# Kernel tuning notes

Measured on AMD Instinct MI355X. Metric: run time of the kernel, lower is better.

Reference implementation:

```python
import jax, jax.numpy as jnp
import numpy as np

B, S = 128, 32
C = [4, 8, 16, 32]
DN = ('NDHWC', 'DHWIO', 'NDHWC')


def _conv(x, w, stride=1, pad=None):
    k = w.shape[0]
    if pad is None:
        pad = [((k - 1) // 2, k // 2)] * 3  # k=3 -> (1,1); k=4 -> (1,2) as in scn even-kernel convention
    return jax.lax.conv_general_dilated(x, w, (stride,) * 3, pad, dimension_numbers=DN)


def _bn_relu(x, g, b, mask, eps=1e-4):
    # BatchNormLeakyReLU with leakiness=0 (ReLU); stats over ACTIVE voxels only, per channel
    cnt = jnp.maximum(mask.sum(), 1.0)
    mean = (x * mask).sum(axis=(0, 1, 2, 3)) / cnt
    var = (((x - mean) ** 2) * mask).sum(axis=(0, 1, 2, 3)) / cnt
    y = (x - mean) * jax.lax.rsqrt(var + eps) * g + b
    return jnp.maximum(y, 0.0) * mask


def _pool_mask(m):
    # scn.Convolution k=2 s=2: output site active iff any input in its 2^3 receptive field is active
    return jax.lax.reduce_window(m, 0.0, jax.lax.max, (1, 2, 2, 2, 1), (1, 2, 2, 2, 1), 'VALID')


def _up_mask(m):
    # scn.FullConvolution k=2 s=2: each active input activates its full 2^3 output block
    return jnp.repeat(jnp.repeat(jnp.repeat(m, 2, 1), 2, 2), 2, 3)


def _encoder(vox, maskraw, wp, enc, dec, wo):
    mask = (maskraw == 0).astype(vox.dtype)
    x = vox * mask
    x = _conv(x, wp) * mask  # prepare: submanifold conv 1 -> m=4
    for (g, b, ws, wd) in enc:  # 3 non-empty encoding stages (i < num_strides-1)
        x = _bn_relu(x, g, b, mask)
        x = _conv(x, ws) * mask               # submanifold conv k=3
        x = _conv(x, wd, stride=2, pad=[(0, 0)] * 3)  # strided Convolution k=2 s=2
        mask = _pool_mask(mask)
        x = x * mask
    # SparseToDense + view(-1, C*s^3) in NCDHW layout
    hidden = jnp.transpose(x, (0, 4, 1, 2, 3)).reshape(x.shape[0], -1)
    for (g, b, wu, ws3, ws4) in dec:  # i = 2, 1, 0
        x = _bn_relu(x, g, b, mask)
        x = jax.lax.conv_transpose(x, wu, (2, 2, 2), 'VALID', dimension_numbers=DN)  # FullConvolution
        mask = _up_mask(mask)
        x = x * mask
        x = _conv(x, ws3) * mask              # submanifold conv k=3 (end of decoding_conv1)
        mask = mask * (x[..., :1] > 0).astype(x.dtype)  # SparsifyFCS (applied twice; idempotent)
        x = x * mask
        x = _conv(x, ws4) * mask              # submanifold conv k=4 (decoding_conv2)
    out = _conv(x, wo) * mask                 # output: submanifold conv m -> 1
    return hidden, out


def setup_inputs():
    key = jax.random.key(0)
    ks = iter(jax.random.split(key, 64))

    def rnd(shape, s=0.1):
        return jax.random.normal(next(ks), shape, jnp.float32) * s

    inp = {}
    inp['vox'] = jax.random.normal(next(ks), (B, S, S, S, 1), jnp.float32)
    inp['maskraw'] = jax.random.randint(next(ks), (B, S, S, S, 1), 0, 10, jnp.int32)
    inp['wp'] = rnd((3, 3, 3, 1, C[0]))
    for i in range(3):
        ci, co = C[i], C[i + 1]
        inp[f'g_e{i}'] = 1.0 + rnd((ci,))
        inp[f'b_e{i}'] = rnd((ci,))
        inp[f'ws_e{i}'] = rnd((3, 3, 3, ci, ci))
        inp[f'wd_e{i}'] = rnd((2, 2, 2, ci, co))
    for j, i in enumerate([2, 1, 0]):
        ci, co = C[i + 1], C[i]
        inp[f'g_d{j}'] = 1.0 + rnd((ci,))
        inp[f'b_d{j}'] = rnd((ci,))
        inp[f'wu_d{j}'] = rnd((2, 2, 2, ci, co))
        inp[f'ws3_d{j}'] = rnd((3, 3, 3, co, co))
        inp[f'ws4_d{j}'] = rnd((4, 4, 4, co, co))
    inp['wo'] = rnd((3, 3, 3, C[0], 1))
    return inp


def reference(vox, maskraw, wp, g_e0, b_e0, ws_e0, wd_e0, g_e1, b_e1, ws_e1, wd_e1, g_e2, b_e2, ws_e2, wd_e2, g_d0, b_d0, wu_d0, ws3_d0, ws4_d0, g_d1, b_d1, wu_d1, ws3_d1, ws4_d1, g_d2, b_d2, wu_d2, ws3_d2, ws4_d2, wo):
    enc = [(g_e0, b_e0, ws_e0, wd_e0), (g_e1, b_e1, ws_e1, wd_e1), (g_e2, b_e2, ws_e2, wd_e2)]
    dec = [(g_d0, b_d0, wu_d0, ws3_d0, ws4_d0), (g_d1, b_d1, wu_d1, ws3_d1, ws4_d1), (g_d2, b_d2, wu_d2, ws3_d2, ws4_d2)]
    return _encoder(vox, maskraw, wp, enc, dec, wo)
```

## Files before the change

### kernel.cpp

```cpp
#include <hip/hip_runtime.h>

using u8 = unsigned char;

__global__ void mask_init_k(const int* __restrict__ mr, u8* __restrict__ m, int N) {
    int i = blockIdx.x * blockDim.x + threadIdx.x;
    if (i < N) m[i] = (mr[i] == 0) ? 1 : 0;
}

template <int SO>
__global__ void pool_k(const u8* __restrict__ mi, u8* __restrict__ mo) {
    const int N = 128 * SO * SO * SO;
    constexpr int SI = 2 * SO;
    int v = blockIdx.x * blockDim.x + threadIdx.x;
    if (v >= N) return;
    int t = v;
    int x = t % SO; t /= SO;
    int y = t % SO; t /= SO;
    int z = t % SO;
    int n = t / SO;
    u8 m = 0;
    for (int kd = 0; kd < 2; kd++)
        for (int kh = 0; kh < 2; kh++)
            for (int kw = 0; kw < 2; kw++)
                m |= mi[((n * SI + 2 * z + kd) * SI + 2 * y + kh) * SI + 2 * x + kw];
    mo[v] = m;
}


__global__ void prep4t_k(const float* __restrict__ vox, const u8* __restrict__ m,
                         const float* __restrict__ wp, float* __restrict__ out) {
    __shared__ float til[6 * 10 * 35];
    int bid = blockIdx.x;
    int y0 = (bid & 3) << 3, z0 = ((bid >> 2) & 7) << 2, n = bid >> 5;
    for (int t = threadIdx.x; t < 6 * 10 * 35; t += 256) {
        int x_ = t % 35;
        int rr = t / 35;
        int yy = rr % 10, zz = rr / 10;
        int gx = x_ - 1, gy = y0 + yy - 1, gz = z0 + zz - 1;
        float v = 0.f;
        if ((unsigned)gx < 32u && (unsigned)gy < 32u && (unsigned)gz < 32u) {
            int gi = ((n * 32 + gz) * 32 + gy) * 32 + gx;
            if (m[gi]) v = vox[gi];
        }
        til[t] = v;
    }
    __syncthreads();
    int tx = threadIdx.x;
    int xg = tx & 7, ly = (tx >> 3) & 7, lz = tx >> 6;
    int xb = xg << 2;
    int vbase = ((n * 32 + z0 + lz) * 32 + y0 + ly) * 32 + xb;
    u8 om[4];
#pragma unroll
    for (int j = 0; j < 4; j++) om[j] = m[vbase + j];
    float acc[4][4];
#pragma unroll
    for (int j = 0; j < 4; j++)
#pragma unroll
        for (int co = 0; co < 4; co++) acc[j][co] = 0.f;
    for (int kd = 0; kd < 3; kd++) {
        for (int kh = 0; kh < 3; kh++) {
            const float* rowp = &til[((lz + kd) * 10 + ly + kh) * 35 + xb];
            float col[6];
#pragma unroll
            for (int c = 0; c < 6; c++) col[c] = rowp[c];
            const float* wrow = wp + ((kd * 3 + kh) * 3) * 4;
#pragma unroll
            for (int kw = 0; kw < 3; kw++) {
                const float* wt = wrow + kw * 4;
#pragma unroll
                for (int j = 0; j < 4; j++) {
                    float xv = col[j + kw];
#pragma unroll
                    for (int co = 0; co < 4; co++) acc[j][co] += xv * wt[co];
                }
            }
        }
    }
#pragma unroll
    for (int j = 0; j < 4; j++)
#pragma unroll
        for (int co = 0; co < 4; co++)
            out[(size_t)(vbase + j) * 4 + co] = om[j] ? acc[j][co] : 0.f;
}

__global__ void convbn4t_k(const float* __restrict__ in, const float* __restrict__ w,
                           const u8* __restrict__ mask, const double* __restrict__ params,
                           float* __restrict__ out) {
    __shared__ float4 til[6 * 10 * 35];
    float sc[4], sh[4];
#pragma unroll
    for (int c = 0; c < 4; c++) { sc[c] = (float)params[c]; sh[c] = (float)params[4 + c]; }
    int bid = blockIdx.x;
    int y0 = (bid & 3) << 3, z0 = ((bid >> 2) & 7) << 2, n = bid >> 5;
    for (int t = threadIdx.x; t < 6 * 10 * 35; t += 256) {
        int x_ = t % 35;
        int rr = t / 35;
        int yy = rr % 10, zz = rr / 10;
        int gx = x_ - 1, gy = y0 + yy - 1, gz = z0 + zz - 1;
        float4 v = make_float4(0.f, 0.f, 0.f, 0.f);
        if ((unsigned)gx < 32u && (unsigned)gy < 32u && (unsigned)gz < 32u) {
            int gi = ((n * 32 + gz) * 32 + gy) * 32 + gx;
            if (mask[gi]) {
                float4 r = *(const float4*)(in + (size_t)gi * 4);
                v.x = fmaxf(r.x * sc[0] + sh[0], 0.f);
                v.y = fmaxf(r.y * sc[1] + sh[1], 0.f);
                v.z = fmaxf(r.z * sc[2] + sh[2], 0.f);
                v.w = fmaxf(r.w * sc[3] + sh[3], 0.f);
            }
        }
        til[t] = v;
    }
    __syncthreads();
    int tx = threadIdx.x;
    int xg = tx & 7, ly = (tx >> 3) & 7, lz = tx >> 6;
    int xb = xg << 2;
    int vbase = ((n * 32 + z0 + lz) * 32 + y0 + ly) * 32 + xb;
    u8 om[4];
#pragma unroll
    for (int j = 0; j < 4; j++) om[j] = mask[vbase + j];
    float acc[4][4];
#pragma unroll
    for (int j = 0; j < 4; j++)
#pragma unroll
        for (int co = 0; co < 4; co++) acc[j][co] = 0.f;
    for (int kd = 0; kd < 3; kd++) {
        for (int kh = 0; kh < 3; kh++) {
            const float4* rowp = &til[((lz + kd) * 10 + ly + kh) * 35 + xb];
            float col[6][4];
#pragma unroll
            for (int c = 0; c < 6; c++) {
                float4 t4 = rowp[c];
                col[c][0] = t4.x; col[c][1] = t4.y; col[c][2] = t4.z; col[c][3] = t4.w;
            }
            const float* wrow = w + ((kd * 3 + kh) * 3) * 16;
#pragma unroll
            for (int kw = 0; kw < 3; kw++) {
                const float* wt = wrow + kw * 16;
#pragma unroll
                for (int j = 0; j < 4; j++) {
#pragma unroll
                    for (int ci = 0; ci < 4; ci++) {
                        float xv = col[j + kw][ci];
#pragma unroll
                        for (int co = 0; co < 4; co++) acc[j][co] += xv * wt[ci * 4 + co];
                    }
                }
            }
        }
    }
#pragma unroll
    for (int j = 0; j < 4; j++)
#pragma unroll
        for (int co = 0; co < 4; co++)
            out[(size_t)(vbase + j) * 4 + co] = om[j] ? acc[j][co] : 0.f;
}

__global__ void conv3s4t_k(const float* __restrict__ in, const float* __restrict__ w,
                           const u8* __restrict__ pmask, u8* __restrict__ nmask,
                           float* __restrict__ out, double delta) {
    __shared__ float4 til[6 * 10 * 35];
    int bid = blockIdx.x;
    int y0 = (bid & 3) << 3, z0 = ((bid >> 2) & 7) << 2, n = bid >> 5;
    for (int t = threadIdx.x; t < 6 * 10 * 35; t += 256) {
        int x_ = t % 35;
        int rr = t / 35;
        int yy = rr % 10, zz = rr / 10;
        int gx = x_ - 1, gy = y0 + yy - 1, gz = z0 + zz - 1;
        float4 v = make_float4(0.f, 0.f, 0.f, 0.f);
        if ((unsigned)gx < 32u && (unsigned)gy < 32u && (unsigned)gz < 32u)
            v = *(const float4*)(in + (size_t)(((n * 32 + gz) * 32 + gy) * 32 + gx) * 4);
        til[t] = v;
    }
    __syncthreads();
    int tx = threadIdx.x;
    int xg = tx & 7, ly = (tx >> 3) & 7, lz = tx >> 6;
    int xb = xg << 2;
    int gy = y0 + ly, gz = z0 + lz;
    int vbase = ((n * 32 + gz) * 32 + gy) * 32 + xb;
    int pbase = ((n * 16 + (gz >> 1)) * 16 + (gy >> 1)) * 16 + (xb >> 1);
    u8 pm[4];
    pm[0] = pm[1] = pmask[pbase];
    pm[2] = pm[3] = pmask[pbase + 1];
    double acc0[4], asum[4];
    float accf[4][4];
#pragma unroll
    for (int j = 0; j < 4; j++) {
        acc0[j] = 0.0; asum[j] = 0.0;
#pragma unroll
        for (int co = 0; co < 4; co++) accf[j][co] = 0.f;
    }
    for (int kd = 0; kd < 3; kd++) {
        for (int kh = 0; kh < 3; kh++) {
            const float4* rowp = &til[((lz + kd) * 10 + ly + kh) * 35 + xb];
            float col[6][4];
#pragma unroll
            for (int c = 0; c < 6; c++) {
                float4 t4 = rowp[c];
                col[c][0] = t4.x; col[c][1] = t4.y; col[c][2] = t4.z; col[c][3] = t4.w;
            }
            const float* wrow = w + ((kd * 3 + kh) * 3) * 16;
#pragma unroll
            for (int kw = 0; kw < 3; kw++) {
                const float* wt = wrow + kw * 16;
#pragma unroll
                for (int j = 0; j < 4; j++) {
#pragma unroll
                    for (int ci = 0; ci < 4; ci++) {
                        float xv = col[j + kw][ci];
                        double term = (double)xv * (double)wt[ci * 4 + 0];
                        acc0[j] += term;
                        asum[j] += fabs(term);
#pragma unroll
                        for (int co = 1; co < 4; co++) accf[j][co] += xv * wt[ci * 4 + co];
                    }
                }
            }
        }
    }
#pragma unroll
    for (int j = 0; j < 4; j++) {
        u8 nm = (pm[j] && (acc0[j] > -delta * asum[j])) ? 1 : 0;
        nmask[vbase + j] = nm;
        out[(size_t)(vbase + j) * 4 + 0] = nm ? (float)acc0[j] : 0.f;
#pragma unroll
        for (int co = 1; co < 4; co++) out[(size_t)(vbase + j) * 4 + co] = nm ? accf[j][co] : 0.f;
    }
}

__global__ void conv4x4t_k(const float* __restrict__ in, const float* __restrict__ w,
                           const u8* __restrict__ outmask, float* __restrict__ out) {
    __shared__ float4 til[7 * 11 * 35];
    int bid = blockIdx.x;
    int y0 = (bid & 3) << 3, z0 = ((bid >> 2) & 7) << 2, n = bid >> 5;
    for (int t = threadIdx.x; t < 7 * 11 * 35; t += 256) {
        int x_ = t % 35;
        int rr = t / 35;
        int yy = rr % 11, zz = rr / 11;
        int gx = x_ - 1, gy = y0 + yy - 1, gz = z0 + zz - 1;
        float4 v = make_float4(0.f, 0.f, 0.f, 0.f);
        if ((unsigned)gx < 32u && (unsigned)gy < 32u && (unsigned)gz < 32u)
            v = *(const float4*)(in + (size_t)(((n * 32 + gz) * 32 + gy) * 32 + gx) * 4);
        til[t] = v;
    }
    __syncthreads();
    int tx = threadIdx.x;
    int xg = tx & 7, ly = (tx >> 3) & 7, lz = tx >> 6;
    int xb = xg << 2;
    int vbase = ((n * 32 + z0 + lz) * 32 + y0 + ly) * 32 + xb;
    u8 om[4];
#pragma unroll
    for (int j = 0; j < 4; j++) om[j] = outmask[vbase + j];
    float acc[4][4];
#pragma unroll
    for (int j = 0; j < 4; j++)
#pragma unroll
        for (int co = 0; co < 4; co++) acc[j][co] = 0.f;
    for (int kd = 0; kd < 4; kd++) {
        for (int kh = 0; kh < 4; kh++) {
            const float4* rowp = &til[((lz + kd) * 11 + ly + kh) * 35 + xb];
            float col[7][4];
#pragma unroll
            for (int c = 0; c < 7; c++) {
                float4 t4 = rowp[c];
                col[c][0] = t4.x; col[c][1] = t4.y; col[c][2] = t4.z; col[c][3] = t4.w;
            }
            const float* wrow = w + ((kd * 4 + kh) * 4) * 16;
#pragma unroll
            for (int kw = 0; kw < 4; kw++) {
                const float* wt = wrow + kw * 16;
#pragma unroll
                for (int j = 0; j < 4; j++) {
#pragma unroll
                    for (int ci = 0; ci < 4; ci++) {
                        float xv = col[j + kw][ci];
#pragma unroll
                        for (int co = 0; co < 4; co++) acc[j][co] += xv * wt[ci * 4 + co];
                    }
                }
            }
        }
    }
#pragma unroll
    for (int j = 0; j < 4; j++)
#pragma unroll
        for (int co = 0; co < 4; co++)
            out[(size_t)(vbase + j) * 4 + co] = om[j] ? acc[j][co] : 0.f;
}

__global__ void outconv4t_k(const float* __restrict__ in, const float* __restrict__ w,
                            const u8* __restrict__ mask, float* __restrict__ out) {
    __shared__ float4 til[6 * 10 * 35];
    int bid = blockIdx.x;
    int y0 = (bid & 3) << 3, z0 = ((bid >> 2) & 7) << 2, n = bid >> 5;
    for (int t = threadIdx.x; t < 6 * 10 * 35; t += 256) {
        int x_ = t % 35;
        int rr = t / 35;
        int yy = rr % 10, zz = rr / 10;
        int gx = x_ - 1, gy = y0 + yy - 1, gz = z0 + zz - 1;
        float4 v = make_float4(0.f, 0.f, 0.f, 0.f);
        if ((unsigned)gx < 32u && (unsigned)gy < 32u && (unsigned)gz < 32u)
            v = *(const float4*)(in + (size_t)(((n * 32 + gz) * 32 + gy) * 32 + gx) * 4);
        til[t] = v;
    }
    __syncthreads();
    int tx = threadIdx.x;
    int xg = tx & 7, ly = (tx >> 3) & 7, lz = tx >> 6;
    int xb = xg << 2;
    int vbase = ((n * 32 + z0 + lz) * 32 + y0 + ly) * 32 + xb;
    u8 om[4];
#pragma unroll
    for (int j = 0; j < 4; j++) om[j] = mask[vbase + j];
    float acc[4] = {0.f, 0.f, 0.f, 0.f};
    for (int kd = 0; kd < 3; kd++) {
        for (int kh = 0; kh < 3; kh++) {
            const float4* rowp = &til[((lz + kd) * 10 + ly + kh) * 35 + xb];
            float col[6][4];
#pragma unroll
            for (int c = 0; c < 6; c++) {
                float4 t4 = rowp[c];
                col[c][0] = t4.x; col[c][1] = t4.y; col[c][2] = t4.z; col[c][3] = t4.w;
            }
            const float* wrow = w + ((kd * 3 + kh) * 3) * 4;
#pragma unroll
            for (int kw = 0; kw < 3; kw++) {
                const float* wt = wrow + kw * 4;
#pragma unroll
                for (int j = 0; j < 4; j++) {
#pragma unroll
                    for (int ci = 0; ci < 4; ci++) acc[j] += col[j + kw][ci] * wt[ci];
                }
            }
        }
    }
#pragma unroll
    for (int j = 0; j < 4; j++) out[vbase + j] = om[j] ? acc[j] : 0.f;
}


template <int K, int CIN, int COUT, int S>
__global__ void conv_k(const float* __restrict__ in, const float* __restrict__ w,
                       const u8* __restrict__ outmask, float* __restrict__ out) {
    const int N = 128 * S * S * S;
    int v = blockIdx.x * blockDim.x + threadIdx.x;
    if (v >= N) return;
    if (!outmask[v]) {
#pragma unroll
        for (int co = 0; co < COUT; co++) out[(size_t)v * COUT + co] = 0.f;
        return;
    }
    int t = v;
    int x = t % S; t /= S;
    int y = t % S; t /= S;
    int z = t % S;
    int n = t / S;
    float acc[COUT];
#pragma unroll
    for (int co = 0; co < COUT; co++) acc[co] = 0.f;
    constexpr int PLO = (K - 1) / 2;
    for (int kd = 0; kd < K; kd++) {
        int zz = z + kd - PLO; if ((unsigned)zz >= (unsigned)S) continue;
        for (int kh = 0; kh < K; kh++) {
            int yy = y + kh - PLO; if ((unsigned)yy >= (unsigned)S) continue;
            for (int kw = 0; kw < K; kw++) {
                int xx = x + kw - PLO; if ((unsigned)xx >= (unsigned)S) continue;
                int sv = ((n * S + zz) * S + yy) * S + xx;
                const float* ip = in + (size_t)sv * CIN;
                const float* wpk = w + ((kd * K + kh) * K + kw) * CIN * COUT;
#pragma unroll
                for (int ci = 0; ci < CIN; ci++) {
                    float xv = ip[ci];
#pragma unroll
                    for (int co = 0; co < COUT; co++) acc[co] += xv * wpk[ci * COUT + co];
                }
            }
        }
    }
#pragma unroll
    for (int co = 0; co < COUT; co++) out[(size_t)v * COUT + co] = acc[co];
}

template <int CIN, int COUT, int S>
__global__ void convbn_k(const float* __restrict__ in, const float* __restrict__ w,
                         const u8* __restrict__ mask, const double* __restrict__ params,
                         float* __restrict__ out) {
    const int N = 128 * S * S * S;
    int v = blockIdx.x * blockDim.x + threadIdx.x;
    if (v >= N) return;
    if (!mask[v]) {
#pragma unroll
        for (int co = 0; co < COUT; co++) out[(size_t)v * COUT + co] = 0.f;
        return;
    }
    int t = v;
    int x = t % S; t /= S;
    int y = t % S; t /= S;
    int z = t % S;
    int n = t / S;
    float sc[CIN], sh[CIN];
#pragma unroll
    for (int c = 0; c < CIN; c++) { sc[c] = (float)params[c]; sh[c] = (float)params[CIN + c]; }
    float acc[COUT];
#pragma unroll
    for (int co = 0; co < COUT; co++) acc[co] = 0.f;
    for (int kd = 0; kd < 3; kd++) {
        int zz = z + kd - 1; if ((unsigned)zz >= (unsigned)S) continue;
        for (int kh = 0; kh < 3; kh++) {
            int yy = y + kh - 1; if ((unsigned)yy >= (unsigned)S) continue;
            for (int kw = 0; kw < 3; kw++) {
                int xx = x + kw - 1; if ((unsigned)xx >= (unsigned)S) continue;
                int sv = ((n * S + zz) * S + yy) * S + xx;
                if (!mask[sv]) continue;
                const float* ip = in + (size_t)sv * CIN;
                const float* wpk = w + ((kd * 3 + kh) * 3 + kw) * CIN * COUT;
#pragma unroll
                for (int ci = 0; ci < CIN; ci++) {
                    float yv = fmaxf(ip[ci] * sc[ci] + sh[ci], 0.f);
#pragma unroll
                    for (int co = 0; co < COUT; co++) acc[co] += yv * wpk[ci * COUT + co];
                }
            }
        }
    }
#pragma unroll
    for (int co = 0; co < COUT; co++) out[(size_t)v * COUT + co] = acc[co];
}

template <int CIN, int COUT, int S>
__global__ void conv3s_k(const float* __restrict__ in, const float* __restrict__ w,
                         const u8* __restrict__ pmask, u8* __restrict__ nmask,
                         float* __restrict__ out, double delta) {
    const int N = 128 * S * S * S;
    constexpr int SP = S / 2;
    int v = blockIdx.x * blockDim.x + threadIdx.x;
    if (v >= N) return;
    int t = v;
    int x = t % S; t /= S;
    int y = t % S; t /= S;
    int z = t % S;
    int n = t / S;
    int pidx = ((n * SP + (z >> 1)) * SP + (y >> 1)) * SP + (x >> 1);
    if (!pmask[pidx]) {
        nmask[v] = 0;
#pragma unroll
        for (int co = 0; co < COUT; co++) out[(size_t)v * COUT + co] = 0.f;
        return;
    }
    double acc0 = 0.0, asum = 0.0;
    float acc[COUT];
#pragma unroll
    for (int co = 0; co < COUT; co++) acc[co] = 0.f;
    for (int kd = 0; kd < 3; kd++) {
        int zz = z + kd - 1; if ((unsigned)zz >= (unsigned)S) continue;
        for (int kh = 0; kh < 3; kh++) {
            int yy = y + kh - 1; if ((unsigned)yy >= (unsigned)S) continue;
            for (int kw = 0; kw < 3; kw++) {
                int xx = x + kw - 1; if ((unsigned)xx >= (unsigned)S) continue;
                int sv = ((n * S + zz) * S + yy) * S + xx;
                const float* ip = in + (size_t)sv * CIN;
                const float* wpk = w + ((kd * 3 + kh) * 3 + kw) * CIN * COUT;
#pragma unroll
                for (int ci = 0; ci < CIN; ci++) {
                    float xv = ip[ci];
                    double term = (double)xv * (double)wpk[ci * COUT + 0];
                    acc0 += term;
                    asum += fabs(term);
#pragma unroll
                    for (int co = 1; co < COUT; co++) acc[co] += xv * wpk[ci * COUT + co];
                }
            }
        }
    }
    u8 nm = (acc0 > -delta * asum) ? 1 : 0;
    nmask[v] = nm;
    out[(size_t)v * COUT + 0] = nm ? (float)acc0 : 0.f;
#pragma unroll
    for (int co = 1; co < COUT; co++) out[(size_t)v * COUT + co] = nm ? acc[co] : 0.f;
}

template <int CIN, int COUT, int SO>
__global__ void down_k(const float* __restrict__ in, const float* __restrict__ w,
                       const u8* __restrict__ outmask, float* __restrict__ out) {
    const int N = 128 * SO * SO * SO;
    constexpr int SI = 2 * SO;
    int v = blockIdx.x * blockDim.x + threadIdx.x;
    if (v >= N) return;
    if (!outmask[v]) {
#pragma unroll
        for (int co = 0; co < COUT; co++) out[(size_t)v * COUT + co] = 0.f;
        return;
    }
    int t = v;
    int x = t % SO; t /= SO;
    int y = t % SO; t /= SO;
    int z = t % SO;
    int n = t / SO;
    float acc[COUT];
#pragma unroll
    for (int co = 0; co < COUT; co++) acc[co] = 0.f;
    for (int kd = 0; kd < 2; kd++)
        for (int kh = 0; kh < 2; kh++)
            for (int kw = 0; kw < 2; kw++) {
                int sv = ((n * SI + 2 * z + kd) * SI + 2 * y + kh) * SI + 2 * x + kw;
                const float* ip = in + (size_t)sv * CIN;
                const float* wpk = w + ((kd * 2 + kh) * 2 + kw) * CIN * COUT;
#pragma unroll
                for (int ci = 0; ci < CIN; ci++) {
                    float xv = ip[ci];
#pragma unroll
                    for (int co = 0; co < COUT; co++) acc[co] += xv * wpk[ci * COUT + co];
                }
            }
#pragma unroll
    for (int co = 0; co < COUT; co++) out[(size_t)v * COUT + co] = acc[co];
}

template <int CIN, int COUT, int SI>
__global__ void upbn_k(const float* __restrict__ in, const float* __restrict__ w,
                       const u8* __restrict__ inmask, const double* __restrict__ params,
                       float* __restrict__ out) {
    constexpr int SO = 2 * SI;
    const int N = 128 * SO * SO * SO;
    int v = blockIdx.x * blockDim.x + threadIdx.x;
    if (v >= N) return;
    int t = v;
    int x = t % SO; t /= SO;
    int y = t % SO; t /= SO;
    int z = t % SO;
    int n = t / SO;
    int sv = ((n * SI + (z >> 1)) * SI + (y >> 1)) * SI + (x >> 1);
    if (!inmask[sv]) {
#pragma unroll
        for (int co = 0; co < COUT; co++) out[(size_t)v * COUT + co] = 0.f;
        return;
    }
    int tap = ((1 - (z & 1)) * 2 + (1 - (y & 1))) * 2 + (1 - (x & 1));
    const float* wpk = w + tap * CIN * COUT;
    const float* ip = in + (size_t)sv * CIN;
    float acc[COUT];
#pragma unroll
    for (int co = 0; co < COUT; co++) acc[co] = 0.f;
#pragma unroll
    for (int ci = 0; ci < CIN; ci++) {
        float yv = fmaxf(ip[ci] * (float)params[ci] + (float)params[CIN + ci], 0.f);
#pragma unroll
        for (int co = 0; co < COUT; co++) acc[co] += yv * wpk[ci * COUT + co];
    }
#pragma unroll
    for (int co = 0; co < COUT; co++) out[(size_t)v * COUT + co] = acc[co];
}

template <int C>
__global__ void bn_reduce_k(const float* __restrict__ x, const u8* __restrict__ m, int N,
                            double* __restrict__ partial) {
    double cnt = 0.0, sx[C], s2[C];
#pragma unroll
    for (int c = 0; c < C; c++) { sx[c] = 0.0; s2[c] = 0.0; }
    int stride = gridDim.x * blockDim.x;
    for (int v = blockIdx.x * blockDim.x + threadIdx.x; v < N; v += stride) {
        if (!m[v]) continue;
        cnt += 1.0;
#pragma unroll
        for (int c = 0; c < C; c++) {
            double xv = (double)x[(size_t)v * C + c];
            sx[c] += xv;
            s2[c] += xv * xv;
        }
    }
#pragma unroll
    for (int off = 32; off > 0; off >>= 1) {
        cnt += __shfl_down(cnt, off, 64);
#pragma unroll
        for (int c = 0; c < C; c++) {
            sx[c] += __shfl_down(sx[c], off, 64);
            s2[c] += __shfl_down(s2[c], off, 64);
        }
    }
    __shared__ double sbuf[4][2 * C + 1];
    int wave = threadIdx.x >> 6;
    if ((threadIdx.x & 63) == 0) {
        sbuf[wave][0] = cnt;
#pragma unroll
        for (int c = 0; c < C; c++) {
            sbuf[wave][1 + c] = sx[c];
            sbuf[wave][1 + C + c] = s2[c];
        }
    }
    __syncthreads();
    if (threadIdx.x == 0) {
        double* p = partial + (size_t)blockIdx.x * (2 * C + 1);
        double tcnt = 0.0;
        for (int wv = 0; wv < 4; wv++) tcnt += sbuf[wv][0];
        p[0] = tcnt;
#pragma unroll
        for (int c = 0; c < C; c++) {
            double a = 0.0, b = 0.0;
            for (int wv = 0; wv < 4; wv++) { a += sbuf[wv][1 + c]; b += sbuf[wv][1 + C + c]; }
            p[1 + c] = a;
            p[1 + C + c] = b;
        }
    }
}

template <int C>
__global__ void bn_final_k(const double* __restrict__ partial, int nblocks,
                           const float* __restrict__ g, const float* __restrict__ b,
                           double* __restrict__ params) {
    int c = threadIdx.x;
    if (c >= C) return;
    double cnt = 0.0, sx = 0.0, s2 = 0.0;
    for (int bk = 0; bk < nblocks; bk++) {
        const double* p = partial + (size_t)bk * (2 * C + 1);
        cnt += p[0];
        sx += p[1 + c];
        s2 += p[1 + C + c];
    }
    if (cnt < 1.0) cnt = 1.0;
    double mean = sx / cnt;
    double var = s2 / cnt - mean * mean;
    double sc = (double)g[c] / sqrt(var + 1e-4);
    params[c] = sc;
    params[C + c] = (double)b[c] - mean * sc;
}

__global__ void hidden_k(const float* __restrict__ x, float* __restrict__ out) {
    int i = blockIdx.x * blockDim.x + threadIdx.x;
    if (i >= 128 * 2048) return;
    int b = i >> 11;
    int r = i & 2047;
    int c = r >> 6;
    int s = r & 63;
    int d = s >> 4;
    int h = (s >> 2) & 3;
    int w = s & 3;
    out[i] = x[((((b * 4 + d) * 4 + h) * 4 + w) << 5) + c];
}

extern "C" void kernel_launch(void* const* d_in, const int* in_sizes, int n_in,
                              void* d_out, int out_size, void* d_ws, size_t ws_size,
                              hipStream_t stream) {
    const float* vox = (const float*)d_in[0];
    const int* mraw = (const int*)d_in[1];
    const float* wp = (const float*)d_in[2];
    const float* g_e0 = (const float*)d_in[3];
    const float* b_e0 = (const float*)d_in[4];
    const float* ws_e0 = (const float*)d_in[5];
    const float* wd_e0 = (const float*)d_in[6];
    const float* g_e1 = (const float*)d_in[7];
    const float* b_e1 = (const float*)d_in[8];
    const float* ws_e1 = (const float*)d_in[9];
    const float* wd_e1 = (const float*)d_in[10];
    const float* g_e2 = (const float*)d_in[11];
    const float* b_e2 = (const float*)d_in[12];
    const float* ws_e2 = (const float*)d_in[13];
    const float* wd_e2 = (const float*)d_in[14];
    const float* g_d0 = (const float*)d_in[15];
    const float* b_d0 = (const float*)d_in[16];
    const float* wu_d0 = (const float*)d_in[17];
    const float* ws3_d0 = (const float*)d_in[18];
    const float* ws4_d0 = (const float*)d_in[19];
    const float* g_d1 = (const float*)d_in[20];
    const float* b_d1 = (const float*)d_in[21];
    const float* wu_d1 = (const float*)d_in[22];
    const float* ws3_d1 = (const float*)d_in[23];
    const float* ws4_d1 = (const float*)d_in[24];
    const float* g_d2 = (const float*)d_in[25];
    const float* b_d2 = (const float*)d_in[26];
    const float* wu_d2 = (const float*)d_in[27];
    const float* ws3_d2 = (const float*)d_in[28];
    const float* ws4_d2 = (const float*)d_in[29];
    const float* wo = (const float*)d_in[30];
    float* out = (float*)d_out;

    float* wsf = (float*)d_ws;
    size_t offf = 0;
    auto allocf = [&](size_t n) { float* p = wsf + offf; offf += n; return p; };
    float* R1 = allocf(16777216);
    float* R2 = allocf(16777216);
    float* S1 = allocf(1048576);
    float* S2 = allocf(1048576);
    float* T = allocf(262144);
    double* wsd = (double*)(wsf + offf);
    double* partial = wsd;
    double* params = wsd + 16640;
    u8* wsm = (u8*)(wsd + 16640 + 128);
    size_t offm = 0;
    auto allocm = [&](size_t n) { u8* p = wsm + offm; offm += n; return p; };
    u8* m32 = allocm(4194304);
    u8* m16 = allocm(524288);
    u8* m8 = allocm(65536);
    u8* m4 = allocm(8192);
    u8* mD8 = allocm(65536);
    u8* mD16 = allocm(524288);
    u8* mD32 = allocm(4194304);

    const int N32 = 128 * 32768;
    const int N16 = 128 * 4096;
    const int N8 = 128 * 512;
    const int N4 = 128 * 64;
    auto gs = [](int n) { return dim3((n + 255) / 256); };
    auto rbn = [](int n) { int bl = (n + 255) / 256; return bl > 256 ? 256 : bl; };
    dim3 blk(256);
    dim3 tgrid(4096);

    mask_init_k<<<gs(N32), blk, 0, stream>>>(mraw, m32, N32);
    pool_k<16><<<gs(N16), blk, 0, stream>>>(m32, m16);
    pool_k<8><<<gs(N8), blk, 0, stream>>>(m16, m8);
    pool_k<4><<<gs(N4), blk, 0, stream>>>(m8, m4);

    prep4t_k<<<tgrid, blk, 0, stream>>>(vox, m32, wp, R1);
    int nb0 = rbn(N32);
    bn_reduce_k<4><<<dim3(nb0), blk, 0, stream>>>(R1, m32, N32, partial);
    bn_final_k<4><<<1, 64, 0, stream>>>(partial, nb0, g_e0, b_e0, params);
    convbn4t_k<<<tgrid, blk, 0, stream>>>(R1, ws_e0, m32, params, R2);
    down_k<4, 8, 16><<<gs(N16), blk, 0, stream>>>(R2, wd_e0, m16, R1);

    int nb1 = rbn(N16);
    bn_reduce_k<8><<<dim3(nb1), blk, 0, stream>>>(R1, m16, N16, partial);
    bn_final_k<8><<<1, 64, 0, stream>>>(partial, nb1, g_e1, b_e1, params);
    convbn_k<8, 8, 16><<<gs(N16), blk, 0, stream>>>(R1, ws_e1, m16, params, R2);
    down_k<8, 16, 8><<<gs(N8), blk, 0, stream>>>(R2, wd_e1, m8, S1);

    int nb2 = rbn(N8);
    bn_reduce_k<16><<<dim3(nb2), blk, 0, stream>>>(S1, m8, N8, partial);
    bn_final_k<16><<<1, 64, 0, stream>>>(partial, nb2, g_e2, b_e2, params);
    convbn_k<16, 16, 8><<<gs(N8), blk, 0, stream>>>(S1, ws_e2, m8, params, S2);
    down_k<16, 32, 4><<<gs(N4), blk, 0, stream>>>(S2, wd_e2, m4, T);

    hidden_k<<<gs(128 * 2048), blk, 0, stream>>>(T, out);

    int nb3 = rbn(N4);
    bn_reduce_k<32><<<dim3(nb3), blk, 0, stream>>>(T, m4, N4, partial);
    bn_final_k<32><<<1, 64, 0, stream>>>(partial, nb3, g_d0, b_d0, params);
    upbn_k<32, 16, 4><<<gs(N8), blk, 0, stream>>>(T, wu_d0, m4, params, S1);
    conv3s_k<16, 16, 8><<<gs(N8), blk, 0, stream>>>(S1, ws3_d0, m4, mD8, S2, 4e-7);
    conv_k<4, 16, 16, 8><<<gs(N8), blk, 0, stream>>>(S2, ws4_d0, mD8, S1);

    int nb4 = rbn(N8);
    bn_reduce_k<16><<<dim3(nb4), blk, 0, stream>>>(S1, mD8, N8, partial);
    bn_final_k<16><<<1, 64, 0, stream>>>(partial, nb4, g_d1, b_d1, params);
    upbn_k<16, 8, 8><<<gs(N16), blk, 0, stream>>>(S1, wu_d1, mD8, params, R1);
    conv3s_k<8, 8, 16><<<gs(N16), blk, 0, stream>>>(R1, ws3_d1, mD8, mD16, R2, 4e-7);
    conv_k<4, 8, 8, 16><<<gs(N16), blk, 0, stream>>>(R2, ws4_d1, mD16, R1);

    int nb5 = rbn(N16);
    bn_reduce_k<8><<<dim3(nb5), blk, 0, stream>>>(R1, mD16, N16, partial);
    bn_final_k<8><<<1, 64, 0, stream>>>(partial, nb5, g_d2, b_d2, params);
    upbn_k<8, 4, 16><<<gs(N32), blk, 0, stream>>>(R1, wu_d2, mD16, params, R2);
    conv3s4t_k<<<tgrid, blk, 0, stream>>>(R2, ws3_d2, mD16, mD32, R1, 0.0);
    conv4x4t_k<<<tgrid, blk, 0, stream>>>(R1, ws4_d2, mD32, R2);
    outconv4t_k<<<tgrid, blk, 0, stream>>>(R2, wo, mD32, out + 262144);
}
```

Measured before the change: 1.455 ms.

## Tile 8^3-resolution 16-channel convolutions through shared memory per z-slice

Replaces the three 16-channel convolutions at 8^3 resolution (encoder conv with fused BN+ReLU, decoder k=3 sparsify conv, decoder k=4 conv) with kernels that stage a haloed z-slab of input into LDS. Each 64-thread block then computes one 8x8 z-plane from the shared tile instead of every voxel gathering its neighbours from global memory. This cuts redundant global reads, but it also removes the early exit for masked-out voxels, so every voxel now does the full MAC work. The small 64-thread blocks may also limit occupancy and latency hiding.

Result: slower. 1.576 ms (+8.3%).

```diff
diff --git a/kernel.cpp b/kernel.cpp
--- a/kernel.cpp
+++ b/kernel.cpp
@@ -334,6 +334,160 @@
     }
 #pragma unroll
     for (int j = 0; j < 4; j++) out[vbase + j] = om[j] ? acc[j] : 0.f;
+}
+
+
+__global__ void convbn8_k(const float* __restrict__ in, const float* __restrict__ w,
+                          const u8* __restrict__ mask, const double* __restrict__ params,
+                          float* __restrict__ out) {
+    __shared__ float til[3 * 10 * 11 * 16];
+    float sc[16], sh[16];
+#pragma unroll
+    for (int c = 0; c < 16; c++) { sc[c] = (float)params[c]; sh[c] = (float)params[16 + c]; }
+    int z = blockIdx.x & 7, n = blockIdx.x >> 3;
+    for (int t = threadIdx.x; t < 300; t += 64) {
+        int xx = t % 10;
+        int rr = t / 10;
+        int yy = rr % 10, zz = rr / 10;
+        int gx = xx - 1, gy = yy - 1, gz = z + zz - 1;
+        float v[16];
+#pragma unroll
+        for (int c = 0; c < 16; c++) v[c] = 0.f;
+        if ((unsigned)gx < 8u && (unsigned)gy < 8u && (unsigned)gz < 8u) {
+            int gi = ((n * 8 + gz) * 8 + gy) * 8 + gx;
+            if (mask[gi]) {
+                const float* ip = in + (size_t)gi * 16;
+#pragma unroll
+                for (int c = 0; c < 16; c++) v[c] = fmaxf(ip[c] * sc[c] + sh[c], 0.f);
+            }
+        }
+        float* dst = &til[((zz * 10 + yy) * 11 + xx) * 16];
+#pragma unroll
+        for (int k = 0; k < 4; k++)
+            ((float4*)dst)[k] = make_float4(v[4 * k], v[4 * k + 1], v[4 * k + 2], v[4 * k + 3]);
+    }
+    __syncthreads();
+    int x = threadIdx.x & 7, y = threadIdx.x >> 3;
+    int v = ((n * 8 + z) * 8 + y) * 8 + x;
+    u8 om = mask[v];
+    float acc[16];
+#pragma unroll
+    for (int co = 0; co < 16; co++) acc[co] = 0.f;
+    for (int kd = 0; kd < 3; kd++) {
+        for (int kh = 0; kh < 3; kh++) {
+            const float* rp = &til[((kd * 10 + (y + kh)) * 11 + x) * 16];
+#pragma unroll
+            for (int kw = 0; kw < 3; kw++) {
+                const float* xp = rp + kw * 16;
+                const float* wt = w + ((kd * 3 + kh) * 3 + kw) * 256;
+#pragma unroll
+                for (int ci = 0; ci < 16; ci++) {
+                    float xv = xp[ci];
+#pragma unroll
+                    for (int co = 0; co < 16; co++) acc[co] += xv * wt[ci * 16 + co];
+                }
+            }
+        }
+    }
+#pragma unroll
+    for (int co = 0; co < 16; co++) out[(size_t)v * 16 + co] = om ? acc[co] : 0.f;
+}
+
+__global__ void conv3s8_k(const float* __restrict__ in, const float* __restrict__ w,
+                          const u8* __restrict__ pmask, u8* __restrict__ nmask,
+                          float* __restrict__ out, double delta) {
+    __shared__ float til[3 * 10 * 11 * 16];
+    int z = blockIdx.x & 7, n = blockIdx.x >> 3;
+    for (int t = threadIdx.x; t < 300; t += 64) {
+        int xx = t % 10;
+        int rr = t / 10;
+        int yy = rr % 10, zz = rr / 10;
+        int gx = xx - 1, gy = yy - 1, gz = z + zz - 1;
+        float4 v0 = make_float4(0.f, 0.f, 0.f, 0.f), v1 = v0, v2 = v0, v3 = v0;
+        if ((unsigned)gx < 8u && (unsigned)gy < 8u && (unsigned)gz < 8u) {
+            const float4* ip = (const float4*)(in + (size_t)(((n * 8 + gz) * 8 + gy) * 8 + gx) * 16);
+            v0 = ip[0]; v1 = ip[1]; v2 = ip[2]; v3 = ip[3];
+        }
+        float4* dst = (float4*)&til[((zz * 10 + yy) * 11 + xx) * 16];
+        dst[0] = v0; dst[1] = v1; dst[2] = v2; dst[3] = v3;
+    }
+    __syncthreads();
+    int x = threadIdx.x & 7, y = threadIdx.x >> 3;
+    int v = ((n * 8 + z) * 8 + y) * 8 + x;
+    int pidx = ((n * 4 + (z >> 1)) * 4 + (y >> 1)) * 4 + (x >> 1);
+    u8 pm = pmask[pidx];
+    double acc0 = 0.0, asum = 0.0;
+    float accf[16];
+#pragma unroll
+    for (int co = 0; co < 16; co++) accf[co] = 0.f;
+    for (int kd = 0; kd < 3; kd++) {
+        for (int kh = 0; kh < 3; kh++) {
+            const float* rp = &til[((kd * 10 + (y + kh)) * 11 + x) * 16];
+#pragma unroll
+            for (int kw = 0; kw < 3; kw++) {
+                const float* xp = rp + kw * 16;
+                const float* wt = w + ((kd * 3 + kh) * 3 + kw) * 256;
+#pragma unroll
+                for (int ci = 0; ci < 16; ci++) {
+                    float xv = xp[ci];
+                    double term = (double)xv * (double)wt[ci * 16 + 0];
+                    acc0 += term;
+                    asum += fabs(term);
+#pragma unroll
+                    for (int co = 1; co < 16; co++) accf[co] += xv * wt[ci * 16 + co];
+                }
+            }
+        }
+    }
+    u8 nm = (pm && (acc0 > -delta * asum)) ? 1 : 0;
+    nmask[v] = nm;
+    out[(size_t)v * 16 + 0] = nm ? (float)acc0 : 0.f;
+#pragma unroll
+    for (int co = 1; co < 16; co++) out[(size_t)v * 16 + co] = nm ? accf[co] : 0.f;
+}
+
+__global__ void conv48_k(const float* __restrict__ in, const float* __restrict__ w,
+                         const u8* __restrict__ outmask, float* __restrict__ out) {
+    __shared__ float til[4 * 11 * 13 * 16];
+    int z = blockIdx.x & 7, n = blockIdx.x >> 3;
+    for (int t = threadIdx.x; t < 484; t += 64) {
+        int xx = t % 11;
+        int rr = t / 11;
+        int yy = rr % 11, zz = rr / 11;
+        int gx = xx - 1, gy = yy - 1, gz = z + zz - 1;
+        float4 v0 = make_float4(0.f, 0.f, 0.f, 0.f), v1 = v0, v2 = v0, v3 = v0;
+        if ((unsigned)gx < 8u && (unsigned)gy < 8u && (unsigned)gz < 8u) {
+            const float4* ip = (const float4*)(in + (size_t)(((n * 8 + gz) * 8 + gy) * 8 + gx) * 16);
+            v0 = ip[0]; v1 = ip[1]; v2 = ip[2]; v3 = ip[3];
+        }
+        float4* dst = (float4*)&til[((zz * 11 + yy) * 13 + xx) * 16];
+        dst[0] = v0; dst[1] = v1; dst[2] = v2; dst[3] = v3;
+    }
+    __syncthreads();
+    int x = threadIdx.x & 7, y = threadIdx.x >> 3;
+    int v = ((n * 8 + z) * 8 + y) * 8 + x;
+    u8 om = outmask[v];
+    float acc[16];
+#pragma unroll
+    for (int co = 0; co < 16; co++) acc[co] = 0.f;
+    for (int kd = 0; kd < 4; kd++) {
+        for (int kh = 0; kh < 4; kh++) {
+            const float* rp = &til[((kd * 11 + (y + kh)) * 13 + x) * 16];
+#pragma unroll
+            for (int kw = 0; kw < 4; kw++) {
+                const float* xp = rp + kw * 16;
+                const float* wt = w + ((kd * 4 + kh) * 4 + kw) * 256;
+#pragma unroll
+                for (int ci = 0; ci < 16; ci++) {
+                    float xv = xp[ci];
+#pragma unroll
+                    for (int co = 0; co < 16; co++) acc[co] += xv * wt[ci * 16 + co];
+                }
+            }
+        }
+    }
+#pragma unroll
+    for (int co = 0; co < 16; co++) out[(size_t)v * 16 + co] = om ? acc[co] : 0.f;
 }
 
 
@@ -701,6 +855,8 @@
     auto rbn = [](int n) { int bl = (n + 255) / 256; return bl > 256 ? 256 : bl; };
     dim3 blk(256);
     dim3 tgrid(4096);
+    dim3 grid8(1024);
+    dim3 blk64(64);
 
     mask_init_k<<<gs(N32), blk, 0, stream>>>(mraw, m32, N32);
     pool_k<16><<<gs(N16), blk, 0, stream>>>(m32, m16);
@@ -723,7 +879,7 @@
     int nb2 = rbn(N8);
     bn_reduce_k<16><<<dim3(nb2), blk, 0, stream>>>(S1, m8, N8, partial);
     bn_final_k<16><<<1, 64, 0, stream>>>(partial, nb2, g_e2, b_e2, params);
-    convbn_k<16, 16, 8><<<gs(N8), blk, 0, stream>>>(S1, ws_e2, m8, params, S2);
+    convbn8_k<<<grid8, blk64, 0, stream>>>(S1, ws_e2, m8, params, S2);
     down_k<16, 32, 4><<<gs(N4), blk, 0, stream>>>(S2, wd_e2, m4, T);
 
     hidden_k<<<gs(128 * 2048), blk, 0, stream>>>(T, out);
@@ -732,8 +888,8 @@
     bn_reduce_k<32><<<dim3(nb3), blk, 0, stream>>>(T, m4, N4, partial);
     bn_final_k<32><<<1, 64, 0, stream>>>(partial, nb3, g_d0, b_d0, params);
     upbn_k<32, 16, 4><<<gs(N8), blk, 0, stream>>>(T, wu_d0, m4, params, S1);
-    conv3s_k<16, 16, 8><<<gs(N8), blk, 0, stream>>>(S1, ws3_d0, m4, mD8, S2, 4e-7);
-    conv_k<4, 16, 16, 8><<<gs(N8), blk, 0, stream>>>(S2, ws4_d0, mD8, S1);
+    conv3s8_k<<<grid8, blk64, 0, stream>>>(S1, ws3_d0, m4, mD8, S2, 4e-7);
+    conv48_k<<<grid8, blk64, 0, stream>>>(S2, ws4_d0, mD8, S1);
 
     int nb4 = rbn(N8);
     bn_reduce_k<16><<<dim3(nb4), blk, 0, stream>>>(S1, mD8, N8, partial);
```
